# Kernel tuning notes

Measured on AMD Instinct MI355X. Metric: run time of the kernel, lower is better.

## Reference

```python
import jax, jax.numpy as jnp
import numpy as np

N = 40000
E = 640000
IN_C = 128
HID = 256
HEADS = 8


def _gat(x, W, att_src, att_dst, bias, src, dst, num_nodes, heads, concat):
    # x: [N, Fin], W: [Fin, heads*C], att_*: [heads, C], bias: [out_dim]
    xp = (x @ W).reshape(num_nodes, heads, -1)          # [N, H, C]
    a_s = jnp.sum(xp * att_src, axis=-1)                # [N, H]
    a_d = jnp.sum(xp * att_dst, axis=-1)                # [N, H]
    e = jax.nn.leaky_relu(a_s[src] + a_d[dst], 0.2)     # [E, H]
    # per-destination-node softmax over incoming edges (self-loops guarantee >=1)
    m = jax.ops.segment_max(e, dst, num_segments=num_nodes)
    m = jnp.where(jnp.isfinite(m), m, 0.0)
    ex = jnp.exp(e - m[dst])
    denom = jax.ops.segment_sum(ex, dst, num_segments=num_nodes)
    alpha = ex / (denom[dst] + 1e-16)                   # [E, H]
    out = jax.ops.segment_sum(xp[src] * alpha[..., None], dst, num_segments=num_nodes)  # [N,H,C]
    out = out.reshape(num_nodes, -1) if concat else out.mean(axis=1)
    return out + bias


def setup_inputs() -> dict:
    key = jax.random.key(0)
    ks = jax.random.split(key, 16)
    C = HID // HEADS
    s = 0.05
    return {
        "x": jax.random.normal(ks[0], (N, IN_C), jnp.float32),
        "edge_index": jax.random.randint(ks[1], (2, E), 0, N, jnp.int32),
        "W0": jax.random.normal(ks[2], (IN_C, HEADS * C), jnp.float32) * s,
        "att_s0": jax.random.normal(ks[3], (HEADS, C), jnp.float32) * s,
        "att_d0": jax.random.normal(ks[4], (HEADS, C), jnp.float32) * s,
        "b0": jnp.zeros((HID,), jnp.float32),
        # BatchNorm(256)
        "gamma0": jnp.ones((HID,), jnp.float32),
        "beta0": jnp.zeros((HID,), jnp.float32),
        # skip projection Linear(128 -> 256)
        "W_skip": jax.random.normal(ks[5], (IN_C, HID), jnp.float32) * s,
        "b_skip": jnp.zeros((HID,), jnp.float32),
        # last layer: GATConv(256 -> 256, heads=1, concat=False)
        "W1": jax.random.normal(ks[6], (HID, HID), jnp.float32) * s,
        "att_s1": jax.random.normal(ks[7], (1, HID), jnp.float32) * s,
        "att_d1": jax.random.normal(ks[8], (1, HID), jnp.float32) * s,
        "b1": jnp.zeros((HID,), jnp.float32),
    }


def reference(x, edge_index, W0, att_s0, att_d0, b0, gamma0, beta0,
              W_skip, b_skip, W1, att_s1, att_d1, b1):
    loops = jnp.arange(N, dtype=edge_index.dtype)
    src = jnp.concatenate([edge_index[0], loops])
    dst = jnp.concatenate([edge_index[1], loops])
    # conv 0 (heads=8, concat)
    h = _gat(x, W0, att_s0, att_d0, b0, src, dst, N, HEADS, True)
    # BatchNorm (training-style batch stats, biased variance, eps=1e-5)
    mu = h.mean(axis=0)
    var = h.var(axis=0)
    h = (h - mu) / jnp.sqrt(var + 1e-5) * gamma0 + beta0
    h = jax.nn.elu(h)
    # dropout is identity in eval mode
    # residual: shapes differ (128 vs 256) -> skip_proj(x_initial) + h at i==0
    h = h + (x @ W_skip + b_skip)
    # conv 1 (heads=1, concat=False -> mean over single head)
    out = _gat(h, W1, att_s1, att_d1, b1, src, dst, N, 1, False)
    return out
```

## Files before the change

kernel.cpp:

```cpp
#include <hip/hip_runtime.h>
#include <hip/hip_bf16.h>

#define NN 40000
#define EE 640000
#define ET 680000
#define MPAD 40064
#define LOG2E 1.4426950408889634f

typedef __attribute__((ext_vector_type(8))) short short8;
typedef __attribute__((ext_vector_type(4))) float f32x4;

__device__ __forceinline__ float bf2f(unsigned u) {
    return __uint_as_float(u << 16);
}
__device__ __forceinline__ unsigned short f2bf(float f) {
    unsigned u = __float_as_uint(f);
    return (unsigned short)((u + 0x7FFFu + ((u >> 16) & 1u)) >> 16);
}
__device__ __forceinline__ unsigned pack2(float lo, float hi) {
    return ((unsigned)f2bf(lo)) | (((unsigned)f2bf(hi)) << 16);
}
__device__ __forceinline__ void unpack2(unsigned u, float& lo, float& hi) {
    lo = __uint_as_float(u << 16);
    hi = __uint_as_float(u & 0xffff0000u);
}

__global__ __launch_bounds__(256) void conv_x(const float* __restrict__ x,
                                              unsigned short* __restrict__ xb)
{
    int i = blockIdx.x * 256 + threadIdx.x;
    if (i >= MPAD * 128 / 4) return;
    int row = (i * 4) >> 7;
    ushort4 o;
    if (row < NN) {
        float4 v = ((const float4*)x)[i];
        o.x = f2bf(v.x); o.y = f2bf(v.y); o.z = f2bf(v.z); o.w = f2bf(v.w);
    } else { o.x = o.y = o.z = o.w = 0; }
    ((ushort4*)xb)[i] = o;
}

__global__ __launch_bounds__(256) void conv_wt_all(
    const float* __restrict__ W0, const float* __restrict__ Ws,
    const float* __restrict__ W1, unsigned short* __restrict__ Wtc,
    unsigned short* __restrict__ W1t)
{
    int i = blockIdx.x * 256 + threadIdx.x;
    if (i < 32768) {
        int c = i >> 7, k = i & 127;
        Wtc[i] = f2bf(W0[(size_t)k * 256 + c]);
    } else if (i < 65536) {
        int j = i - 32768;
        int c = j >> 7, k = j & 127;
        Wtc[i] = f2bf(Ws[(size_t)k * 256 + c]);
    } else if (i < 131072) {
        int j = i - 65536;
        int c = j >> 8, k = j & 255;
        W1t[j] = f2bf(W1[(size_t)k * 256 + c]);
    }
}

__global__ __launch_bounds__(256) void gemm_bf16(
    const unsigned short* __restrict__ A, const unsigned short* __restrict__ Btc,
    unsigned short* __restrict__ C0, unsigned short* __restrict__ C1, int K)
{
    __shared__ unsigned short As[128 * 64];
    int tid = threadIdx.x;
    int rb = blockIdx.x * 128, cb = blockIdx.y * 128;
    int lane = tid & 63, wid = tid >> 6;
    int wm = (wid >> 1) * 64, wn = (wid & 1) * 64;
    int lr = lane & 15, lk = lane >> 4;
    f32x4 acc[4][4] = {};
    for (int kb = 0; kb < K; kb += 64) {
        #pragma unroll
        for (int i = 0; i < 4; i++) {
            int flat = tid + i * 256;
            int r = flat >> 3, c8 = flat & 7;
            int4 v = *(const int4*)(A + (size_t)(rb + r) * K + kb + c8 * 8);
            *(int4*)(&As[r * 64 + ((c8 ^ (r & 7)) * 8)]) = v;
        }
        __syncthreads();
        #pragma unroll
        for (int kk = 0; kk < 2; kk++) {
            int kbase = kb + kk * 32 + lk * 8;
            short8 bfr[4], afr[4];
            #pragma unroll
            for (int n = 0; n < 4; n++)
                bfr[n] = *(const short8*)(Btc + (size_t)(cb + wn + n * 16 + lr) * K + kbase);
            #pragma unroll
            for (int m = 0; m < 4; m++) {
                int row = wm + m * 16 + lr;
                int kchunk = kk * 4 + lk;
                afr[m] = *(const short8*)(&As[row * 64 + ((kchunk ^ (row & 7)) * 8)]);
            }
            #pragma unroll
            for (int m = 0; m < 4; m++)
                #pragma unroll
                for (int n = 0; n < 4; n++)
                    acc[m][n] = __builtin_amdgcn_mfma_f32_16x16x32_bf16(afr[m], bfr[n], acc[m][n], 0, 0, 0);
        }
        __syncthreads();
    }
    unsigned short* C = (cb < 256) ? C0 : C1;
    int cbase = cb & 255;
    #pragma unroll
    for (int m = 0; m < 4; m++)
        #pragma unroll
        for (int n = 0; n < 4; n++) {
            int col = cbase + wn + n * 16 + lr;
            #pragma unroll
            for (int j = 0; j < 4; j++) {
                int row = rb + wm + m * 16 + lk * 4 + j;
                C[(size_t)row * 256 + col] = f2bf(acc[m][n][j]);
            }
        }
}

__global__ __launch_bounds__(256) void csr_count(const int* __restrict__ ei, int* __restrict__ deg)
{
    int e = blockIdx.x * blockDim.x + threadIdx.x;
    if (e >= ET) return;
    int d = (e < EE) ? ei[EE + e] : (e - EE);
    atomicAdd(&deg[d], 1);
}

__global__ __launch_bounds__(1024) void exscan(
    const int* __restrict__ deg, int* __restrict__ rowptr, int* __restrict__ cursor)
{
    __shared__ int wsum[16];
    __shared__ int carry_s;
    int tid = threadIdx.x, lane = tid & 63, wid = tid >> 6;
    if (tid == 0) carry_s = 0;
    __syncthreads();
    for (int base = 0; base < NN; base += 1024) {
        int i = base + tid;
        int v = (i < NN) ? deg[i] : 0;
        int sc = v;
        #pragma unroll
        for (int off = 1; off < 64; off <<= 1) {
            int t = __shfl_up(sc, off);
            if (lane >= off) sc += t;
        }
        if (lane == 63) wsum[wid] = sc;
        __syncthreads();
        if (wid == 0 && lane < 16) {
            int t = wsum[lane];
            #pragma unroll
            for (int off = 1; off < 16; off <<= 1) {
                int u = __shfl_up(t, off);
                if (lane >= off) t += u;
            }
            wsum[lane] = t;
        }
        __syncthreads();
        int carry = carry_s;
        int wpre = wid ? wsum[wid - 1] : 0;
        int excl = carry + wpre + sc - v;
        if (i < NN) { rowptr[i] = excl; cursor[i] = excl; }
        __syncthreads();
        if (tid == 0) carry_s = carry + wsum[15];
    }
    if (tid == 0) rowptr[NN] = carry_s;
}

__global__ __launch_bounds__(256) void csr_fill(
    const int* __restrict__ ei, int* __restrict__ cursor, int* __restrict__ adj)
{
    int e = blockIdx.x * blockDim.x + threadIdx.x;
    if (e >= ET) return;
    int s, d;
    if (e < EE) { s = ei[e]; d = ei[EE + e]; } else { s = d = e - EE; }
    int pos = atomicAdd(&cursor[d], 1);
    adj[pos] = s;
}

__global__ __launch_bounds__(256) void attn_node0(
    const unsigned short* __restrict__ xp, const float* __restrict__ att_s,
    const float* __restrict__ att_d, float* __restrict__ a_s, float* __restrict__ a_d)
{
    int t = blockIdx.x * 256 + threadIdx.x;
    if (t >= NN * 8) return;
    int n = t >> 3, h = t & 7;
    const unsigned short* p = xp + (size_t)n * 256 + h * 32;
    float s = 0.f, dd = 0.f;
    #pragma unroll
    for (int i0 = 0; i0 < 32; i0 += 8) {
        uint4 raw = *(const uint4*)(p + i0);
        unsigned vals[4] = {raw.x, raw.y, raw.z, raw.w};
        #pragma unroll
        for (int q = 0; q < 4; q++) {
            float lo, hi;
            unpack2(vals[q], lo, hi);
            s  += lo * att_s[h * 32 + i0 + q * 2] + hi * att_s[h * 32 + i0 + q * 2 + 1];
            dd += lo * att_d[h * 32 + i0 + q * 2] + hi * att_d[h * 32 + i0 + q * 2 + 1];
        }
    }
    a_s[t] = s * LOG2E; a_d[t] = dd * LOG2E;
}

__global__ __launch_bounds__(256) void attn_node1(
    const unsigned short* __restrict__ xp, const float* __restrict__ att_s,
    const float* __restrict__ att_d, float* __restrict__ a_s, float* __restrict__ a_d)
{
    int w = (blockIdx.x * 256 + threadIdx.x) >> 6;
    int lane = threadIdx.x & 63;
    if (w >= NN) return;
    ushort4 raw = ((const ushort4*)(xp + (size_t)w * 256))[lane];
    float4 a = ((const float4*)att_s)[lane];
    float4 b = ((const float4*)att_d)[lane];
    float v0 = bf2f(raw.x), v1 = bf2f(raw.y), v2 = bf2f(raw.z), v3 = bf2f(raw.w);
    float s  = v0 * a.x + v1 * a.y + v2 * a.z + v3 * a.w;
    float dd = v0 * b.x + v1 * b.y + v2 * b.z + v3 * b.w;
    #pragma unroll
    for (int off = 32; off; off >>= 1) {
        s  += __shfl_down(s, off);
        dd += __shfl_down(dd, off);
    }
    if (lane == 0) { a_s[w] = s * LOG2E; a_d[w] = dd * LOG2E; }
}

__global__ __launch_bounds__(256) void gather0(
    const int* __restrict__ adj, const int* __restrict__ rowptr,
    const unsigned short* __restrict__ xp, const float* __restrict__ a_s,
    const float* __restrict__ a_d, unsigned short* __restrict__ out0)
{
    int w = (blockIdx.x * 256 + threadIdx.x) >> 6;
    int lane = threadIdx.x & 63;
    if (w >= NN) return;
    int hl = lane & 31;
    int hw = lane >> 5;
    int h = hl >> 2;
    float ad = a_d[w * 8 + h];
    int p = rowptr[w], end = rowptr[w + 1];
    unsigned loff = (unsigned)hl * 16u;
    float a0=0,a1=0,a2=0,a3=0,a4=0,a5=0,a6=0,a7=0;
    float b0=0,b1=0,b2=0,b3=0,b4=0,b5=0,b6=0,b7=0;
    float den0 = 0.f, den1 = 0.f;
    float lo, hi;
    for (; p + 8 <= end; p += 8) {
        int sA = adj[p + hw];
        int sB = adj[p + 2 + hw];
        int sC = adj[p + 4 + hw];
        int sD = adj[p + 6 + hw];
        float eA = a_s[sA * 8 + h] + ad;
        float eB = a_s[sB * 8 + h] + ad;
        float eC = a_s[sC * 8 + h] + ad;
        float eD = a_s[sD * 8 + h] + ad;
        float wA = __builtin_amdgcn_exp2f(fmaxf(eA, 0.2f * eA));
        float wB = __builtin_amdgcn_exp2f(fmaxf(eB, 0.2f * eB));
        float wC = __builtin_amdgcn_exp2f(fmaxf(eC, 0.2f * eC));
        float wD = __builtin_amdgcn_exp2f(fmaxf(eD, 0.2f * eD));
        uint4 rA = *(const uint4*)((const char*)xp + ((unsigned)sA * 512u + loff));
        uint4 rB = *(const uint4*)((const char*)xp + ((unsigned)sB * 512u + loff));
        uint4 rC = *(const uint4*)((const char*)xp + ((unsigned)sC * 512u + loff));
        uint4 rD = *(const uint4*)((const char*)xp + ((unsigned)sD * 512u + loff));
        den0 += wA + wC; den1 += wB + wD;
        unpack2(rA.x, lo, hi); a0 += wA * lo; a1 += wA * hi;
        unpack2(rA.y, lo, hi); a2 += wA * lo; a3 += wA * hi;
        unpack2(rA.z, lo, hi); a4 += wA * lo; a5 += wA * hi;
        unpack2(rA.w, lo, hi); a6 += wA * lo; a7 += wA * hi;
        unpack2(rB.x, lo, hi); b0 += wB * lo; b1 += wB * hi;
        unpack2(rB.y, lo, hi); b2 += wB * lo; b3 += wB * hi;
        unpack2(rB.z, lo, hi); b4 += wB * lo; b5 += wB * hi;
        unpack2(rB.w, lo, hi); b6 += wB * lo; b7 += wB * hi;
        unpack2(rC.x, lo, hi); a0 += wC * lo; a1 += wC * hi;
        unpack2(rC.y, lo, hi); a2 += wC * lo; a3 += wC * hi;
        unpack2(rC.z, lo, hi); a4 += wC * lo; a5 += wC * hi;
        unpack2(rC.w, lo, hi); a6 += wC * lo; a7 += wC * hi;
        unpack2(rD.x, lo, hi); b0 += wD * lo; b1 += wD * hi;
        unpack2(rD.y, lo, hi); b2 += wD * lo; b3 += wD * hi;
        unpack2(rD.z, lo, hi); b4 += wD * lo; b5 += wD * hi;
        unpack2(rD.w, lo, hi); b6 += wD * lo; b7 += wD * hi;
    }
    for (; p + 2 <= end; p += 2) {
        int sA = adj[p + hw];
        float eA = a_s[sA * 8 + h] + ad;
        float wA = __builtin_amdgcn_exp2f(fmaxf(eA, 0.2f * eA));
        uint4 rA = *(const uint4*)((const char*)xp + ((unsigned)sA * 512u + loff));
        den0 += wA;
        unpack2(rA.x, lo, hi); a0 += wA * lo; a1 += wA * hi;
        unpack2(rA.y, lo, hi); a2 += wA * lo; a3 += wA * hi;
        unpack2(rA.z, lo, hi); a4 += wA * lo; a5 += wA * hi;
        unpack2(rA.w, lo, hi); a6 += wA * lo; a7 += wA * hi;
    }
    if (p < end) {
        int sA = adj[p];
        float eA = a_s[sA * 8 + h] + ad;
        float wA = hw ? 0.f : __builtin_amdgcn_exp2f(fmaxf(eA, 0.2f * eA));
        uint4 rA = *(const uint4*)((const char*)xp + ((unsigned)sA * 512u + loff));
        den0 += wA;
        unpack2(rA.x, lo, hi); a0 += wA * lo; a1 += wA * hi;
        unpack2(rA.y, lo, hi); a2 += wA * lo; a3 += wA * hi;
        unpack2(rA.z, lo, hi); a4 += wA * lo; a5 += wA * hi;
        unpack2(rA.w, lo, hi); a6 += wA * lo; a7 += wA * hi;
    }
    a0 += b0; a1 += b1; a2 += b2; a3 += b3;
    a4 += b4; a5 += b5; a6 += b6; a7 += b7;
    float den = den0 + den1;
    den += __shfl_xor(den, 32);
    a0 += __shfl_xor(a0, 32); a1 += __shfl_xor(a1, 32);
    a2 += __shfl_xor(a2, 32); a3 += __shfl_xor(a3, 32);
    a4 += __shfl_xor(a4, 32); a5 += __shfl_xor(a5, 32);
    a6 += __shfl_xor(a6, 32); a7 += __shfl_xor(a7, 32);
    if (hw == 0) {
        float inv = 1.f / (den + 1e-16f);
        uint4 o;
        o.x = pack2(a0 * inv, a1 * inv);
        o.y = pack2(a2 * inv, a3 * inv);
        o.z = pack2(a4 * inv, a5 * inv);
        o.w = pack2(a6 * inv, a7 * inv);
        *(uint4*)((char*)out0 + ((size_t)w * 512u + loff)) = o;
    }
}

__global__ __launch_bounds__(256) void bn_stats(
    const unsigned short* __restrict__ H, float* __restrict__ bnsum, float* __restrict__ bnsq)
{
    int c = threadIdx.x;
    int r0 = blockIdx.x * 64;
    float s = 0.f, sq = 0.f;
    for (int r = r0; r < r0 + 64; r++) {
        float v = bf2f(H[(size_t)r * 256 + c]);
        s += v; sq += v * v;
    }
    atomicAdd(&bnsum[c], s);
    atomicAdd(&bnsq[c], sq);
}

__global__ __launch_bounds__(256) void bn_elu(
    const unsigned short* __restrict__ out0, unsigned short* __restrict__ hb,
    const float* __restrict__ bnsum, const float* __restrict__ bnsq,
    const float* __restrict__ gamma, const float* __restrict__ beta,
    const float* __restrict__ bskip)
{
    int i = blockIdx.x * 256 + threadIdx.x;
    if (i >= MPAD * 256 / 8) return;
    int col0 = (i * 8) & 255;
    uint4 hv = ((const uint4*)out0)[i];
    uint4 sv = ((const uint4*)hb)[i];
    float bn[8], sk[8];
    unpack2(hv.x, bn[0], bn[1]); unpack2(hv.y, bn[2], bn[3]);
    unpack2(hv.z, bn[4], bn[5]); unpack2(hv.w, bn[6], bn[7]);
    unpack2(sv.x, sk[0], sk[1]); unpack2(sv.y, sk[2], sk[3]);
    unpack2(sv.z, sk[4], sk[5]); unpack2(sv.w, sk[6], sk[7]);
    const float invN = 1.0f / (float)NN;
    float r[8];
    #pragma unroll
    for (int q = 0; q < 8; q++) {
        int c = col0 + q;
        float mu = bnsum[c] * invN;
        float var = bnsq[c] * invN - mu * mu;
        float scl = rsqrtf(var + 1e-5f) * gamma[c];
        float b = (bn[q] - mu) * scl + beta[c];
        float el = b > 0.f ? b : (__expf(b) - 1.f);
        r[q] = el + sk[q] + bskip[c];
    }
    uint4 o;
    o.x = pack2(r[0], r[1]); o.y = pack2(r[2], r[3]);
    o.z = pack2(r[4], r[5]); o.w = pack2(r[6], r[7]);
    ((uint4*)hb)[i] = o;
}

__global__ __launch_bounds__(256) void gather1(
    const int* __restrict__ adj, const int* __restrict__ rowptr,
    const unsigned short* __restrict__ xp, const float* __restrict__ a_s,
    const float* __restrict__ a_d, const float* __restrict__ b1,
    float* __restrict__ out)
{
    int w = (blockIdx.x * 256 + threadIdx.x) >> 6;
    int lane = threadIdx.x & 63;
    if (w >= NN) return;
    int hl = lane & 31;
    int hw = lane >> 5;
    float ad = a_d[w];
    int p = rowptr[w], end = rowptr[w + 1];
    unsigned loff = (unsigned)hl * 16u;
    float a0=0,a1=0,a2=0,a3=0,a4=0,a5=0,a6=0,a7=0;
    float b0s=0,b1s=0,b2s=0,b3s=0,b4s=0,b5s=0,b6s=0,b7s=0;
    float den0 = 0.f, den1 = 0.f;
    float lo, hi;
    for (; p + 8 <= end; p += 8) {
        int sA = adj[p + hw];
        int sB = adj[p + 2 + hw];
        int sC = adj[p + 4 + hw];
        int sD = adj[p + 6 + hw];
        float eA = a_s[sA] + ad;
        float eB = a_s[sB] + ad;
        float eC = a_s[sC] + ad;
        float eD = a_s[sD] + ad;
        float wA = __builtin_amdgcn_exp2f(fmaxf(eA, 0.2f * eA));
        float wB = __builtin_amdgcn_exp2f(fmaxf(eB, 0.2f * eB));
        float wC = __builtin_amdgcn_exp2f(fmaxf(eC, 0.2f * eC));
        float wD = __builtin_amdgcn_exp2f(fmaxf(eD, 0.2f * eD));
        uint4 rA = *(const uint4*)((const char*)xp + ((unsigned)sA * 512u + loff));
        uint4 rB = *(const uint4*)((const char*)xp + ((unsigned)sB * 512u + loff));
        uint4 rC = *(const uint4*)((const char*)xp + ((unsigned)sC * 512u + loff));
        uint4 rD = *(const uint4*)((const char*)xp + ((unsigned)sD * 512u + loff));
        den0 += wA + wC; den1 += wB + wD;
        unpack2(rA.x, lo, hi); a0 += wA * lo; a1 += wA * hi;
        unpack2(rA.y, lo, hi); a2 += wA * lo; a3 += wA * hi;
        unpack2(rA.z, lo, hi); a4 += wA * lo; a5 += wA * hi;
        unpack2(rA.w, lo, hi); a6 += wA * lo; a7 += wA * hi;
        unpack2(rB.x, lo, hi); b0s += wB * lo; b1s += wB * hi;
        unpack2(rB.y, lo, hi); b2s += wB * lo; b3s += wB * hi;
        unpack2(rB.z, lo, hi); b4s += wB * lo; b5s += wB * hi;
        unpack2(rB.w, lo, hi); b6s += wB * lo; b7s += wB * hi;
        unpack2(rC.x, lo, hi); a0 += wC * lo; a1 += wC * hi;
        unpack2(rC.y, lo, hi); a2 += wC * lo; a3 += wC * hi;
        unpack2(rC.z, lo, hi); a4 += wC * lo; a5 += wC * hi;
        unpack2(rC.w, lo, hi); a6 += wC * lo; a7 += wC * hi;
        unpack2(rD.x, lo, hi); b0s += wD * lo; b1s += wD * hi;
        unpack2(rD.y, lo, hi); b2s += wD * lo; b3s += wD * hi;
        unpack2(rD.z, lo, hi); b4s += wD * lo; b5s += wD * hi;
        unpack2(rD.w, lo, hi); b6s += wD * lo; b7s += wD * hi;
    }
    for (; p + 2 <= end; p += 2) {
        int sA = adj[p + hw];
        float eA = a_s[sA] + ad;
        float wA = __builtin_amdgcn_exp2f(fmaxf(eA, 0.2f * eA));
        uint4 rA = *(const uint4*)((const char*)xp + ((unsigned)sA * 512u + loff));
        den0 += wA;
        unpack2(rA.x, lo, hi); a0 += wA * lo; a1 += wA * hi;
        unpack2(rA.y, lo, hi); a2 += wA * lo; a3 += wA * hi;
        unpack2(rA.z, lo, hi); a4 += wA * lo; a5 += wA * hi;
        unpack2(rA.w, lo, hi); a6 += wA * lo; a7 += wA * hi;
    }
    if (p < end) {
        int sA = adj[p];
        float eA = a_s[sA] + ad;
        float wA = hw ? 0.f : __builtin_amdgcn_exp2f(fmaxf(eA, 0.2f * eA));
        uint4 rA = *(const uint4*)((const char*)xp + ((unsigned)sA * 512u + loff));
        den0 += wA;
        unpack2(rA.x, lo, hi); a0 += wA * lo; a1 += wA * hi;
        unpack2(rA.y, lo, hi); a2 += wA * lo; a3 += wA * hi;
        unpack2(rA.z, lo, hi); a4 += wA * lo; a5 += wA * hi;
        unpack2(rA.w, lo, hi); a6 += wA * lo; a7 += wA * hi;
    }
    a0 += b0s; a1 += b1s; a2 += b2s; a3 += b3s;
    a4 += b4s; a5 += b5s; a6 += b6s; a7 += b7s;
    float den = den0 + den1;
    den += __shfl_xor(den, 32);
    a0 += __shfl_xor(a0, 32); a1 += __shfl_xor(a1, 32);
    a2 += __shfl_xor(a2, 32); a3 += __shfl_xor(a3, 32);
    a4 += __shfl_xor(a4, 32); a5 += __shfl_xor(a5, 32);
    a6 += __shfl_xor(a6, 32); a7 += __shfl_xor(a7, 32);
    if (hw == 0) {
        float inv = 1.f / (den + 1e-16f);
        const float* bb = b1 + hl * 8;
        float4 o0 = {a0 * inv + bb[0], a1 * inv + bb[1],
                     a2 * inv + bb[2], a3 * inv + bb[3]};
        float4 o1 = {a4 * inv + bb[4], a5 * inv + bb[5],
                     a6 * inv + bb[6], a7 * inv + bb[7]};
        float* orow = out + (size_t)w * 256 + hl * 8;
        *(float4*)(orow) = o0;
        *(float4*)(orow + 4) = o1;
    }
}

extern "C" void kernel_launch(void* const* d_in, const int* in_sizes, int n_in,
                              void* d_out, int out_size, void* d_ws, size_t ws_size,
                              hipStream_t stream)
{
    const float* x      = (const float*)d_in[0];
    const int*   ei     = (const int*)d_in[1];
    const float* W0     = (const float*)d_in[2];
    const float* att_s0 = (const float*)d_in[3];
    const float* att_d0 = (const float*)d_in[4];
    const float* gamma0 = (const float*)d_in[6];
    const float* beta0  = (const float*)d_in[7];
    const float* W_skip = (const float*)d_in[8];
    const float* b_skip = (const float*)d_in[9];
    const float* W1     = (const float*)d_in[10];
    const float* att_s1 = (const float*)d_in[11];
    const float* att_d1 = (const float*)d_in[12];
    const float* b1     = (const float*)d_in[13];
    float* out = (float*)d_out;

    char* p = (char*)d_ws;
    unsigned short* x_bf  = (unsigned short*)p; p += (size_t)MPAD * 128 * 2;
    unsigned short* xp_bf = (unsigned short*)p; p += (size_t)MPAD * 256 * 2;
    unsigned short* h_bf  = (unsigned short*)p; p += (size_t)MPAD * 256 * 2;
    unsigned short* out0b = (unsigned short*)p; p += (size_t)MPAD * 256 * 2;
    unsigned short* Wtc   = (unsigned short*)p; p += (size_t)512 * 128 * 2;
    unsigned short* W1t   = (unsigned short*)p; p += (size_t)256 * 256 * 2;
    float* a_s   = (float*)p; p += (size_t)NN * 8 * 4;
    float* a_d   = (float*)p; p += (size_t)NN * 8 * 4;
    float* bnsum = (float*)p; p += 256 * 4;
    float* bnsq  = (float*)p; p += 256 * 4;
    int* deg    = (int*)p; p += (size_t)NN * 4;
    int* rowptr = (int*)p; p += (size_t)(NN + 1) * 4;
    int* cursor = (int*)p; p += (size_t)NN * 4;
    int* adj    = (int*)p; p += (size_t)ET * 4;

    hipMemsetAsync(deg, 0, (size_t)NN * 4, stream);
    hipMemsetAsync(bnsum, 0, 512 * 4, stream);
    hipMemsetAsync(out0b + (size_t)NN * 256, 0, (size_t)(MPAD - NN) * 256 * 2, stream);

    conv_x<<<(MPAD * 128 / 4 + 255) / 256, 256, 0, stream>>>(x, x_bf);
    conv_wt_all<<<(131072 + 255) / 256, 256, 0, stream>>>(W0, W_skip, W1, Wtc, W1t);

    csr_count<<<(ET + 255) / 256, 256, 0, stream>>>(ei, deg);
    exscan<<<1, 1024, 0, stream>>>(deg, rowptr, cursor);
    csr_fill<<<(ET + 255) / 256, 256, 0, stream>>>(ei, cursor, adj);

    dim3 gg0(MPAD / 128, 4);
    gemm_bf16<<<gg0, 256, 0, stream>>>(x_bf, Wtc, xp_bf, h_bf, 128);
    attn_node0<<<(NN * 8 + 255) / 256, 256, 0, stream>>>(xp_bf, att_s0, att_d0, a_s, a_d);
    gather0<<<(NN * 64 + 255) / 256, 256, 0, stream>>>(adj, rowptr, xp_bf, a_s, a_d, out0b);

    bn_stats<<<NN / 64, 256, 0, stream>>>(out0b, bnsum, bnsq);
    bn_elu<<<(MPAD * 256 / 8 + 255) / 256, 256, 0, stream>>>(out0b, h_bf, bnsum, bnsq,
                                                             gamma0, beta0, b_skip);

    dim3 gg1(MPAD / 128, 2);
    gemm_bf16<<<gg1, 256, 0, stream>>>(h_bf, W1t, xp_bf, xp_bf, 256);
    attn_node1<<<(NN * 64 + 255) / 256, 256, 0, stream>>>(xp_bf, att_s1, att_d1, a_s, a_d);
    gather1<<<(NN * 64 + 255) / 256, 256, 0, stream>>>(adj, rowptr, xp_bf, a_s, a_d, b1, out);
}
```

Measured before the change: 321.6 us.

## Schedule gather warps by descending node degree and shrink inner unroll

Adds a counting sort of nodes by in-degree (histogram, scan and permutation fill) so the gather kernels process high-degree destination nodes first. Blocks then hold warps with similar degrees, which is meant to cut intra-block imbalance and tail effects. The main gather loop unroll also drops from 8 edges to 4 per iteration, which lowers register pressure but exposes fewer loads in flight. It adds three small kernels plus a memset, and output writes become scattered rather than sequential.

New measurement: 548.0 us. 1.7x slower.

```diff
diff --git a/kernel.cpp b/kernel.cpp
--- a/kernel.cpp
+++ b/kernel.cpp
@@ -173,6 +173,52 @@
     adj[pos] = s;
 }
 
+__global__ __launch_bounds__(256) void deg_hist(const int* __restrict__ deg,
+                                                int* __restrict__ hist)
+{
+    int n = blockIdx.x * 256 + threadIdx.x;
+    if (n >= NN) return;
+    int b = 511 - min(deg[n], 511);
+    atomicAdd(&hist[b], 1);
+}
+
+__global__ __launch_bounds__(512) void hist_scan(const int* __restrict__ hist,
+                                                 int* __restrict__ bincur)
+{
+    __shared__ int wsum[8];
+    int tid = threadIdx.x, lane = tid & 63, wid = tid >> 6;
+    int v = hist[tid], sc = v;
+    #pragma unroll
+    for (int off = 1; off < 64; off <<= 1) {
+        int t = __shfl_up(sc, off);
+        if (lane >= off) sc += t;
+    }
+    if (lane == 63) wsum[wid] = sc;
+    __syncthreads();
+    if (wid == 0 && lane < 8) {
+        int t = wsum[lane];
+        #pragma unroll
+        for (int off = 1; off < 8; off <<= 1) {
+            int u = __shfl_up(t, off);
+            if (lane >= off) t += u;
+        }
+        wsum[lane] = t;
+    }
+    __syncthreads();
+    bincur[tid] = (wid ? wsum[wid - 1] : 0) + sc - v;
+}
+
+__global__ __launch_bounds__(256) void perm_fill(const int* __restrict__ deg,
+                                                 int* __restrict__ bincur,
+                                                 int* __restrict__ perm)
+{
+    int n = blockIdx.x * 256 + threadIdx.x;
+    if (n >= NN) return;
+    int b = 511 - min(deg[n], 511);
+    int pos = atomicAdd(&bincur[b], 1);
+    perm[pos] = n;
+}
+
 __global__ __launch_bounds__(256) void attn_node0(
     const unsigned short* __restrict__ xp, const float* __restrict__ att_s,
     const float* __restrict__ att_d, float* __restrict__ a_s, float* __restrict__ a_d)
@@ -219,13 +265,15 @@
 }
 
 __global__ __launch_bounds__(256) void gather0(
-    const int* __restrict__ adj, const int* __restrict__ rowptr,
-    const unsigned short* __restrict__ xp, const float* __restrict__ a_s,
-    const float* __restrict__ a_d, unsigned short* __restrict__ out0)
-{
-    int w = (blockIdx.x * 256 + threadIdx.x) >> 6;
+    const int* __restrict__ perm, const int* __restrict__ adj,
+    const int* __restrict__ rowptr, const unsigned short* __restrict__ xp,
+    const float* __restrict__ a_s, const float* __restrict__ a_d,
+    unsigned short* __restrict__ out0)
+{
+    int wi = (blockIdx.x * 256 + threadIdx.x) >> 6;
     int lane = threadIdx.x & 63;
-    if (w >= NN) return;
+    if (wi >= NN) return;
+    int w = perm[wi];
     int hl = lane & 31;
     int hw = lane >> 5;
     int h = hl >> 2;
@@ -236,24 +284,16 @@
     float b0=0,b1=0,b2=0,b3=0,b4=0,b5=0,b6=0,b7=0;
     float den0 = 0.f, den1 = 0.f;
     float lo, hi;
-    for (; p + 8 <= end; p += 8) {
+    for (; p + 4 <= end; p += 4) {
         int sA = adj[p + hw];
         int sB = adj[p + 2 + hw];
-        int sC = adj[p + 4 + hw];
-        int sD = adj[p + 6 + hw];
         float eA = a_s[sA * 8 + h] + ad;
         float eB = a_s[sB * 8 + h] + ad;
-        float eC = a_s[sC * 8 + h] + ad;
-        float eD = a_s[sD * 8 + h] + ad;
         float wA = __builtin_amdgcn_exp2f(fmaxf(eA, 0.2f * eA));
         float wB = __builtin_amdgcn_exp2f(fmaxf(eB, 0.2f * eB));
-        float wC = __builtin_amdgcn_exp2f(fmaxf(eC, 0.2f * eC));
-        float wD = __builtin_amdgcn_exp2f(fmaxf(eD, 0.2f * eD));
         uint4 rA = *(const uint4*)((const char*)xp + ((unsigned)sA * 512u + loff));
         uint4 rB = *(const uint4*)((const char*)xp + ((unsigned)sB * 512u + loff));
-        uint4 rC = *(const uint4*)((const char*)xp + ((unsigned)sC * 512u + loff));
-        uint4 rD = *(const uint4*)((const char*)xp + ((unsigned)sD * 512u + loff));
-        den0 += wA + wC; den1 += wB + wD;
+        den0 += wA; den1 += wB;
         unpack2(rA.x, lo, hi); a0 += wA * lo; a1 += wA * hi;
         unpack2(rA.y, lo, hi); a2 += wA * lo; a3 += wA * hi;
         unpack2(rA.z, lo, hi); a4 += wA * lo; a5 += wA * hi;
@@ -262,14 +302,6 @@
         unpack2(rB.y, lo, hi); b2 += wB * lo; b3 += wB * hi;
         unpack2(rB.z, lo, hi); b4 += wB * lo; b5 += wB * hi;
         unpack2(rB.w, lo, hi); b6 += wB * lo; b7 += wB * hi;
-        unpack2(rC.x, lo, hi); a0 += wC * lo; a1 += wC * hi;
-        unpack2(rC.y, lo, hi); a2 += wC * lo; a3 += wC * hi;
-        unpack2(rC.z, lo, hi); a4 += wC * lo; a5 += wC * hi;
-        unpack2(rC.w, lo, hi); a6 += wC * lo; a7 += wC * hi;
-        unpack2(rD.x, lo, hi); b0 += wD * lo; b1 += wD * hi;
-        unpack2(rD.y, lo, hi); b2 += wD * lo; b3 += wD * hi;
-        unpack2(rD.z, lo, hi); b4 += wD * lo; b5 += wD * hi;
-        unpack2(rD.w, lo, hi); b6 += wD * lo; b7 += wD * hi;
     }
     for (; p + 2 <= end; p += 2) {
         int sA = adj[p + hw];
@@ -361,14 +393,15 @@
 }
 
 __global__ __launch_bounds__(256) void gather1(
-    const int* __restrict__ adj, const int* __restrict__ rowptr,
-    const unsigned short* __restrict__ xp, const float* __restrict__ a_s,
-    const float* __restrict__ a_d, const float* __restrict__ b1,
-    float* __restrict__ out)
-{
-    int w = (blockIdx.x * 256 + threadIdx.x) >> 6;
+    const int* __restrict__ perm, const int* __restrict__ adj,
+    const int* __restrict__ rowptr, const unsigned short* __restrict__ xp,
+    const float* __restrict__ a_s, const float* __restrict__ a_d,
+    const float* __restrict__ b1, float* __restrict__ out)
+{
+    int wi = (blockIdx.x * 256 + threadIdx.x) >> 6;
     int lane = threadIdx.x & 63;
-    if (w >= NN) return;
+    if (wi >= NN) return;
+    int w = perm[wi];
     int hl = lane & 31;
     int hw = lane >> 5;
     float ad = a_d[w];
@@ -378,24 +411,16 @@
     float b0s=0,b1s=0,b2s=0,b3s=0,b4s=0,b5s=0,b6s=0,b7s=0;
     float den0 = 0.f, den1 = 0.f;
     float lo, hi;
-    for (; p + 8 <= end; p += 8) {
+    for (; p + 4 <= end; p += 4) {
         int sA = adj[p + hw];
         int sB = adj[p + 2 + hw];
-        int sC = adj[p + 4 + hw];
-        int sD = adj[p + 6 + hw];
         float eA = a_s[sA] + ad;
         float eB = a_s[sB] + ad;
-        float eC = a_s[sC] + ad;
-        float eD = a_s[sD] + ad;
         float wA = __builtin_amdgcn_exp2f(fmaxf(eA, 0.2f * eA));
         float wB = __builtin_amdgcn_exp2f(fmaxf(eB, 0.2f * eB));
-        float wC = __builtin_amdgcn_exp2f(fmaxf(eC, 0.2f * eC));
-        float wD = __builtin_amdgcn_exp2f(fmaxf(eD, 0.2f * eD));
         uint4 rA = *(const uint4*)((const char*)xp + ((unsigned)sA * 512u + loff));
         uint4 rB = *(const uint4*)((const char*)xp + ((unsigned)sB * 512u + loff));
-        uint4 rC = *(const uint4*)((const char*)xp + ((unsigned)sC * 512u + loff));
-        uint4 rD = *(const uint4*)((const char*)xp + ((unsigned)sD * 512u + loff));
-        den0 += wA + wC; den1 += wB + wD;
+        den0 += wA; den1 += wB;
         unpack2(rA.x, lo, hi); a0 += wA * lo; a1 += wA * hi;
         unpack2(rA.y, lo, hi); a2 += wA * lo; a3 += wA * hi;
         unpack2(rA.z, lo, hi); a4 += wA * lo; a5 += wA * hi;
@@ -404,14 +429,6 @@
         unpack2(rB.y, lo, hi); b2s += wB * lo; b3s += wB * hi;
         unpack2(rB.z, lo, hi); b4s += wB * lo; b5s += wB * hi;
         unpack2(rB.w, lo, hi); b6s += wB * lo; b7s += wB * hi;
-        unpack2(rC.x, lo, hi); a0 += wC * lo; a1 += wC * hi;
-        unpack2(rC.y, lo, hi); a2 += wC * lo; a3 += wC * hi;
-        unpack2(rC.z, lo, hi); a4 += wC * lo; a5 += wC * hi;
-        unpack2(rC.w, lo, hi); a6 += wC * lo; a7 += wC * hi;
-        unpack2(rD.x, lo, hi); b0s += wD * lo; b1s += wD * hi;
-        unpack2(rD.y, lo, hi); b2s += wD * lo; b3s += wD * hi;
-        unpack2(rD.z, lo, hi); b4s += wD * lo; b5s += wD * hi;
-        unpack2(rD.w, lo, hi); b6s += wD * lo; b7s += wD * hi;
     }
     for (; p + 2 <= end; p += 2) {
         int sA = adj[p + hw];
@@ -490,9 +507,13 @@
     int* rowptr = (int*)p; p += (size_t)(NN + 1) * 4;
     int* cursor = (int*)p; p += (size_t)NN * 4;
     int* adj    = (int*)p; p += (size_t)ET * 4;
+    int* hist   = (int*)p; p += 512 * 4;
+    int* bincur = (int*)p; p += 512 * 4;
+    int* perm   = (int*)p; p += (size_t)NN * 4;
 
     hipMemsetAsync(deg, 0, (size_t)NN * 4, stream);
     hipMemsetAsync(bnsum, 0, 512 * 4, stream);
+    hipMemsetAsync(hist, 0, 512 * 4, stream);
     hipMemsetAsync(out0b + (size_t)NN * 256, 0, (size_t)(MPAD - NN) * 256 * 2, stream);
 
     conv_x<<<(MPAD * 128 / 4 + 255) / 256, 256, 0, stream>>>(x, x_bf);
@@ -501,11 +522,15 @@
     csr_count<<<(ET + 255) / 256, 256, 0, stream>>>(ei, deg);
     exscan<<<1, 1024, 0, stream>>>(deg, rowptr, cursor);
     csr_fill<<<(ET + 255) / 256, 256, 0, stream>>>(ei, cursor, adj);
+    deg_hist<<<(NN + 255) / 256, 256, 0, stream>>>(deg, hist);
+    hist_scan<<<1, 512, 0, stream>>>(hist, bincur);
+    perm_fill<<<(NN + 255) / 256, 256, 0, stream>>>(deg, bincur, perm);
 
     dim3 gg0(MPAD / 128, 4);
     gemm_bf16<<<gg0, 256, 0, stream>>>(x_bf, Wtc, xp_bf, h_bf, 128);
     attn_node0<<<(NN * 8 + 255) / 256, 256, 0, stream>>>(xp_bf, att_s0, att_d0, a_s, a_d);
-    gather0<<<(NN * 64 + 255) / 256, 256, 0, stream>>>(adj, rowptr, xp_bf, a_s, a_d, out0b);
+    gather0<<<(NN * 64 + 255) / 256, 256, 0, stream>>>(perm, adj, rowptr, xp_bf,
+                                                       a_s, a_d, out0b);
 
     bn_stats<<<NN / 64, 256, 0, stream>>>(out0b, bnsum, bnsq);
     bn_elu<<<(MPAD * 256 / 8 + 255) / 256, 256, 0, stream>>>(out0b, h_bf, bnsum, bnsq,
@@ -514,5 +539,6 @@
     dim3 gg1(MPAD / 128, 2);
     gemm_bf16<<<gg1, 256, 0, stream>>>(h_bf, W1t, xp_bf, xp_bf, 256);
     attn_node1<<<(NN * 64 + 255) / 256, 256, 0, stream>>>(xp_bf, att_s1, att_d1, a_s, a_d);
-    gather1<<<(NN * 64 + 255) / 256, 256, 0, stream>>>(adj, rowptr, xp_bf, a_s, a_d, b1, out);
-}
+    gather1<<<(NN * 64 + 255) / 256, 256, 0, stream>>>(perm, adj, rowptr, xp_bf,
+                                                       a_s, a_d, b1, out);
+}
```
